# Optimization experiments

Hardware: AMD Instinct MI355X
Metric: run time of the kernel (lower is better)

Reference implementation:

```python
import jax, jax.numpy as jnp
import numpy as np

B, T, DIM = 2, 2048, 2048
H, DH = 16, 128
QC, KVC = 512, 512
DD = 64  # decoupled rope dim


def _rope_freqs(t, dd, theta=10000.0):
    inv = 1.0 / (theta ** (np.arange(0, dd, 2, dtype=np.float32) / dd))  # [dd/2]
    ang = np.arange(t, dtype=np.float32)[:, None] * inv[None, :]         # [T, dd/2]
    return jnp.asarray(np.stack([np.cos(ang), np.sin(ang)], axis=-1))    # [T, dd/2, 2]


def setup_inputs() -> dict:
    key = jax.random.key(0)
    ks = jax.random.split(key, 10)
    def w(k, i, o):
        return jax.random.normal(k, (i, o), jnp.float32) / np.sqrt(i)
    x = jax.random.normal(ks[0], (B, T, DIM), jnp.float32)
    freqs_cis = _rope_freqs(T, DD)
    neg = jnp.float32(-1e9)
    mask = jnp.where(jnp.tril(jnp.ones((T, T), bool)), 0.0, neg).astype(jnp.float32)
    return {
        "x": x, "freqs_cis": freqs_cis, "mask": mask,
        "W_dq": w(ks[1], DIM, QC), "W_uq": w(ks[2], QC, H * DH),
        "W_dkv": w(ks[3], DIM, KVC), "W_uk": w(ks[4], KVC, H * DH),
        "W_uv": w(ks[5], KVC, H * DH), "W_qr": w(ks[6], QC, H * DD),
        "W_kr": w(ks[7], DIM, DD), "W_o": w(ks[8], H * DH, DIM),
    }


def _apply_rope(t, freqs_cis):
    # t: [B, T, H, DD]; freqs_cis: [T, DD/2, 2]
    tp = t.reshape(*t.shape[:-1], -1, 2)               # [B,T,H,DD/2,2]
    cos = freqs_cis[None, :, None, :, 0]
    sin = freqs_cis[None, :, None, :, 1]
    x1, x2 = tp[..., 0], tp[..., 1]
    rot = jnp.stack([x1 * cos - x2 * sin, x1 * sin + x2 * cos], axis=-1)
    return rot.reshape(t.shape)


def reference(x, freqs_cis, mask, W_dq, W_uq, W_dkv, W_uk, W_uv, W_qr, W_kr, W_o):
    q_c = x @ W_dq                                     # [B,T,QC]
    kv_c = x @ W_dkv                                   # [B,T,KVC]
    q_rope = (q_c @ W_qr).reshape(B, T, H, DD)
    kv_rope = jnp.broadcast_to((x @ W_kr)[:, :, None, :], (B, T, H, DD))
    q_rope = _apply_rope(q_rope, freqs_cis)
    kv_rope = _apply_rope(kv_rope, freqs_cis)
    q = (q_c @ W_uq).reshape(B, T, H, DH)
    k = (kv_c @ W_uk).reshape(B, T, H, DH)
    v = (kv_c @ W_uv).reshape(B, T, H, DH)
    q = jnp.concatenate([q, q_rope], axis=-1)          # [B,T,H,DH+DD]
    k = jnp.concatenate([k, kv_rope], axis=-1)
    scale = 1.0 / np.sqrt(DH + DD)
    scores = jnp.einsum("bqhd,bkhd->bhqk", q, k) * scale + mask[None, None]
    attn = jax.nn.softmax(scores, axis=-1)
    out = jnp.einsum("bhqk,bkhd->bqhd", attn, v).reshape(B, T, H * DH)
    return out @ W_o
```

## Files before the change

### kernel.cpp

```cpp
#include <hip/hip_runtime.h>
#include <hip/hip_bf16.h>
#include <cstdint>
#include <cstddef>

typedef __bf16 bf16_t;
typedef __attribute__((ext_vector_type(8))) __bf16 bf16x8;
typedef __attribute__((ext_vector_type(4))) __bf16 bf16x4;
typedef __attribute__((ext_vector_type(4))) float f32x4;

#define B_ 2
#define T_ 2048
#define DIM_ 2048
#define H_ 16
#define DH_ 128
#define DD_ 64
#define DQK_ 192
#define QSTRIDE_ 3072
#define BT_ 4096

__device__ __forceinline__ void gload16(const void* g, void* lds) {
  __builtin_amdgcn_global_load_lds(
      (const __attribute__((address_space(1))) unsigned int*)g,
      (__attribute__((address_space(3))) unsigned int*)lds, 16, 0, 0);
}

struct bf16_4 { bf16_t a, b, c, d; };
__global__ void cast_f32_bf16(const float* __restrict__ in, bf16_t* __restrict__ out, int n4) {
  int i = blockIdx.x * blockDim.x + threadIdx.x;
  if (i >= n4) return;
  float4 v = ((const float4*)in)[i];
  bf16_4 r{(bf16_t)v.x, (bf16_t)v.y, (bf16_t)v.z, (bf16_t)v.w};
  ((bf16_4*)out)[i] = r;
}

__global__ void transpose_all(const float* __restrict__ Wdq, const float* __restrict__ Wdkv,
                              const float* __restrict__ Wkr, const float* __restrict__ Wuq,
                              const float* __restrict__ Wqr, const float* __restrict__ Wuk,
                              const float* __restrict__ Wuv, const float* __restrict__ Wo,
                              bf16_t* __restrict__ Bt1, bf16_t* __restrict__ Bt2,
                              bf16_t* __restrict__ Bt3, bf16_t* __restrict__ Wo_t) {
  __shared__ float tile[32][33];
  int id = blockIdx.x;
  const float* W; bf16_t* Wt; int K, N, Np, kt;
  if (id < 1024)      { W = Wdq;  Wt = Bt1;                          K = 2048; N = 512;  Np = 512;  kt = 64; }
  else if (id < 2048) { W = Wdkv; Wt = Bt1 + (size_t)512 * 2048;  id -= 1024; K = 2048; N = 512;  Np = 512;  kt = 64; }
  else if (id < 2304) { W = Wkr;  Wt = Bt1 + (size_t)1024 * 2048; id -= 2048; K = 2048; N = 64;   Np = 128;  kt = 64; }
  else if (id < 3328) { W = Wuq;  Wt = Bt2;                       id -= 2304; K = 512;  N = 2048; Np = 2048; kt = 16; }
  else if (id < 3840) { W = Wqr;  Wt = Bt2 + (size_t)2048 * 512;  id -= 3328; K = 512;  N = 1024; Np = 1024; kt = 16; }
  else if (id < 4864) { W = Wuk;  Wt = Bt3;                       id -= 3840; K = 512;  N = 2048; Np = 2048; kt = 16; }
  else if (id < 5888) { W = Wuv;  Wt = Bt3 + (size_t)2048 * 512;  id -= 4864; K = 512;  N = 2048; Np = 2048; kt = 16; }
  else                { W = Wo;   Wt = Wo_t;                      id -= 5888; K = 2048; N = 2048; Np = 2048; kt = 64; }
  int k0 = (id % kt) * 32, n0 = (id / kt) * 32;
  int tx = threadIdx.x, ty = threadIdx.y;
#pragma unroll
  for (int i = 0; i < 4; ++i) {
    int k = k0 + ty + i * 8, n = n0 + tx;
    float v = (k < K && n < N) ? W[(size_t)k * N + n] : 0.f;
    tile[ty + i * 8][tx] = v;
  }
  __syncthreads();
#pragma unroll
  for (int i = 0; i < 4; ++i) {
    int n = n0 + ty + i * 8, k = k0 + tx;
    if (n < Np && k < K) Wt[(size_t)n * K + k] = (bf16_t)tile[tx][ty + i * 8];
  }
}

__global__ void transpose_v(const bf16_t* __restrict__ V, bf16_t* __restrict__ Vt) {
  __shared__ bf16_t tile[64 * 64];
  int id = blockIdx.x;
  int t0 = (id & 31) * 64;
  int d0 = ((id >> 5) & 1) * 64;
  int bh = id >> 6;
  int b = bh >> 4, h = bh & 15;
  int t = threadIdx.x;
#pragma unroll
  for (int it = 0; it < 2; ++it) {
    int idx = it * 256 + t;
    int tt = idx >> 3, c = idx & 7;
    bf16x8 v = *(const bf16x8*)&V[(size_t)(b * T_ + t0 + tt) * 2048 + h * 128 + d0 + c * 8];
    int sw = (tt ^ (tt >> 3)) & 7;
    *(bf16x8*)((char*)tile + tt * 128 + 16 * (c ^ sw)) = v;
  }
  __syncthreads();
#pragma unroll
  for (int it = 0; it < 2; ++it) {
    int idx = it * 256 + t;
    int dr = idx >> 3, c = idx & 7;
    bf16_t tmp[8];
#pragma unroll
    for (int u = 0; u < 8; ++u) {
      int sw = (u ^ c) & 7;
      tmp[u] = *(const bf16_t*)((const char*)tile + (8 * c + u) * 128 + ((2 * dr) ^ (16 * sw)));
    }
    *(bf16x8*)&Vt[((size_t)bh * 128 + d0 + dr) * T_ + t0 + c * 8] = *(bf16x8*)tmp;
  }
}

template <int MODE>
__global__ __launch_bounds__(256) void gemm_bt(const bf16_t* __restrict__ A,
                                               const bf16_t* __restrict__ Bt,
                                               void* __restrict__ C0v,
                                               void* __restrict__ C1v,
                                               void* __restrict__ C2v,
                                               const float* __restrict__ fr,
                                               int M, int N, int K, int ldc) {
  __shared__ bf16_t As[128 * 32];
  __shared__ bf16_t Bs[128 * 32];
  const int t = threadIdx.x;
  const int w = t >> 6, l = t & 63, l15 = l & 15, lhi = l >> 4;
  const int m0 = blockIdx.y * 128, n0 = blockIdx.x * 128;
  const int wr = (w >> 1) * 64, wc = (w & 1) * 64;

  f32x4 zero = {0.f, 0.f, 0.f, 0.f};
  f32x4 acc[4][4];
#pragma unroll
  for (int m = 0; m < 4; ++m)
#pragma unroll
    for (int n = 0; n < 4; ++n) acc[m][n] = zero;

  const int e0 = t * 8;
  const int r0 = e0 >> 5, c0 = e0 & 31;
  const int e1 = 2048 + t * 8;
  const int r1 = e1 >> 5, c1 = e1 & 31;

  for (int k0 = 0; k0 < K; k0 += 32) {
    gload16(A + (size_t)(m0 + r0) * K + k0 + c0, &As[e0]);
    gload16(A + (size_t)(m0 + r1) * K + k0 + c1, &As[e1]);
    gload16(Bt + (size_t)(n0 + r0) * K + k0 + c0, &Bs[e0]);
    gload16(Bt + (size_t)(n0 + r1) * K + k0 + c1, &Bs[e1]);
    __syncthreads();
    bf16x8 af[4], bfr[4];
#pragma unroll
    for (int m = 0; m < 4; ++m)
      af[m] = *(const bf16x8*)&As[(wr + m * 16 + l15) * 32 + lhi * 8];
#pragma unroll
    for (int n = 0; n < 4; ++n)
      bfr[n] = *(const bf16x8*)&Bs[(wc + n * 16 + l15) * 32 + lhi * 8];
#pragma unroll
    for (int m = 0; m < 4; ++m)
#pragma unroll
      for (int n = 0; n < 4; ++n)
        acc[m][n] = __builtin_amdgcn_mfma_f32_16x16x32_bf16(af[m], bfr[n], acc[m][n], 0, 0, 0);
    __syncthreads();
  }

#pragma unroll
  for (int m = 0; m < 4; ++m) {
#pragma unroll
    for (int n = 0; n < 4; ++n) {
#pragma unroll
      for (int r = 0; r < 4; ++r) {
        int row = m0 + wr + m * 16 + lhi * 4 + r;
        int col = n0 + wc + n * 16 + l15;
        float v = acc[m][n][r];
        if (MODE == 1) {
          ((float*)C0v)[(size_t)row * ldc + col] = v;
        } else if (MODE == 3) {
          if (col < 512)       ((bf16_t*)C0v)[(size_t)row * 512 + col] = (bf16_t)v;
          else if (col < 1024) ((bf16_t*)C1v)[(size_t)row * 512 + (col - 512)] = (bf16_t)v;
          else if (col < 1088) ((bf16_t*)C2v)[(size_t)row * 64 + (col - 1024)] = (bf16_t)v;
        } else if (MODE == 4) {
          if (col < 2048) {
            ((bf16_t*)C0v)[(size_t)row * QSTRIDE_ + (col >> 7) * DQK_ + (col & 127)] = (bf16_t)v;
          } else {
            float other = __shfl_xor(v, 1, 64);
            int tt = row & (T_ - 1);
            int j = (col & 63) >> 1;
            float2 cs = ((const float2*)fr)[tt * 32 + j];
            float o = (col & 1) ? (other * cs.y + v * cs.x) : (v * cs.x - other * cs.y);
            int hh = (col - 2048) >> 6;
            ((bf16_t*)C0v)[(size_t)row * QSTRIDE_ + hh * DQK_ + 128 + (col & 63)] = (bf16_t)o;
          }
        } else if (MODE == 5) {
          if (col < 2048) ((bf16_t*)C0v)[(size_t)row * QSTRIDE_ + (col >> 7) * DQK_ + (col & 127)] = (bf16_t)v;
          else            ((bf16_t*)C1v)[(size_t)row * 2048 + (col - 2048)] = (bf16_t)v;
        }
      }
    }
  }
}

__global__ void rope_k(const bf16_t* __restrict__ kr, const float* __restrict__ fr,
                       bf16_t* __restrict__ Kb) {
  int idx = blockIdx.x * 256 + threadIdx.x;
  int j = idx & 31;
  int row = idx >> 5;
  int tt = row & (T_ - 1);
  float x1 = (float)kr[(size_t)row * 64 + 2 * j];
  float x2 = (float)kr[(size_t)row * 64 + 2 * j + 1];
  float c = fr[tt * 64 + 2 * j], s = fr[tt * 64 + 2 * j + 1];
  union { bf16_t h2[2]; unsigned u; } pk;
  pk.h2[0] = (bf16_t)(x1 * c - x2 * s);
  pk.h2[1] = (bf16_t)(x1 * s + x2 * c);
#pragma unroll
  for (int h = 0; h < H_; ++h) {
    *(unsigned*)&Kb[(size_t)row * QSTRIDE_ + h * DQK_ + 128 + 2 * j] = pk.u;
  }
}

#define KLDB 200
#define VLDB 72
#define PLDB 68

__global__ __launch_bounds__(256, 2) void flash_attn3(const bf16_t* __restrict__ Q,
                                                      const bf16_t* __restrict__ Kb,
                                                      const bf16_t* __restrict__ Vt,
                                                      bf16_t* __restrict__ Ob) {
  __shared__ bf16_t Ks[64 * KLDB];
  __shared__ bf16_t Vs[128 * VLDB];
  __shared__ bf16_t Ps[4][16 * PLDB];

  const int t = threadIdx.x, w = t >> 6, l = t & 63, l15 = l & 15, lhi = l >> 4;
  const int id = blockIdx.x;
  const int xcd = id & 7, sub = id >> 3;
  const int bh = xcd * 4 + (sub >> 4);
  const int qp = sub & 15;
  const int b = bh >> 4, h = bh & 15;
  const int qa = qp, qb = 31 - qp;
  const float scale = 0.07216878364870322f;

  int rK[6], cK[6];
#pragma unroll
  for (int i = 0; i < 6; ++i) { int idx = i * 256 + t; rK[i] = idx / 24; cK[i] = idx % 24; }
  const int rVt = t >> 3, cV = t & 7;
  const bf16_t* kbase = Kb + (size_t)b * T_ * QSTRIDE_ + h * DQK_;
  const bf16_t* vbase = Vt + (size_t)bh * DH_ * T_;

  bf16x8 kreg[6], vreg[4];
#define LOAD_TILE(K0)                                                                      \
  do {                                                                                     \
    _Pragma("unroll") for (int i = 0; i < 6; ++i)                                          \
        kreg[i] = *(const bf16x8*)(kbase + (size_t)((K0) + rK[i]) * QSTRIDE_ + cK[i] * 8); \
    _Pragma("unroll") for (int i = 0; i < 4; ++i)                                          \
        vreg[i] = *(const bf16x8*)(vbase + (size_t)(i * 32 + rVt) * T_ + (K0) + cV * 8);   \
  } while (0)
#define WRITE_TILE()                                                                       \
  do {                                                                                     \
    _Pragma("unroll") for (int i = 0; i < 6; ++i)                                          \
        *(bf16x8*)&Ks[rK[i] * KLDB + cK[i] * 8] = kreg[i];                                 \
    _Pragma("unroll") for (int i = 0; i < 4; ++i)                                          \
        *(bf16x8*)&Vs[(i * 32 + rVt) * VLDB + cV * 8] = vreg[i];                           \
  } while (0)

  f32x4 zero = {0.f, 0.f, 0.f, 0.f};

  LOAD_TILE(0);
  WRITE_TILE();
  __syncthreads();

  for (int pass = 0; pass < 2; ++pass) {
    const int qt = pass ? qb : qa;

    bf16x8 qf[6];
    {
      const bf16_t* qrow = Q + ((size_t)(b * T_ + qt * 64 + w * 16 + l15)) * QSTRIDE_ + h * DQK_;
#pragma unroll
      for (int kc = 0; kc < 6; ++kc) qf[kc] = *(const bf16x8*)(qrow + kc * 32 + lhi * 8);
    }

    float m_r[4], l_r[4];
    f32x4 accO[8];
#pragma unroll
    for (int r = 0; r < 4; ++r) { m_r[r] = -1e30f; l_r[r] = 0.f; }
#pragma unroll
    for (int n = 0; n < 8; ++n) accO[n] = zero;

    for (int kt = 0; kt <= qt; ++kt) {
      const bool last = (kt == qt);
      const bool haveNext = !(pass == 1 && last);
      if (haveNext) LOAD_TILE(last ? 0 : (kt + 1) * 64);

      f32x4 s[4];
#pragma unroll
      for (int n = 0; n < 4; ++n) s[n] = zero;
      __builtin_amdgcn_s_setprio(1);
#pragma unroll
      for (int kc = 0; kc < 6; ++kc) {
#pragma unroll
        for (int n = 0; n < 4; ++n) {
          bf16x8 kf = *(const bf16x8*)&Ks[(n * 16 + l15) * KLDB + kc * 32 + lhi * 8];
          s[n] = __builtin_amdgcn_mfma_f32_16x16x32_bf16(qf[kc], kf, s[n], 0, 0, 0);
        }
      }
      __builtin_amdgcn_s_setprio(0);

#pragma unroll
      for (int n = 0; n < 4; ++n)
#pragma unroll
        for (int r = 0; r < 4; ++r) {
          float v = s[n][r] * scale;
          if (last) {
            int qq = w * 16 + lhi * 4 + r;
            int kk = n * 16 + l15;
            if (kk > qq) v = -1e30f;
          }
          s[n][r] = v;
        }
      float mn[4], corr[4];
#pragma unroll
      for (int r = 0; r < 4; ++r) {
        float v = fmaxf(fmaxf(s[0][r], s[1][r]), fmaxf(s[2][r], s[3][r]));
#pragma unroll
        for (int off = 1; off < 16; off <<= 1) v = fmaxf(v, __shfl_xor(v, off, 64));
        mn[r] = fmaxf(m_r[r], v);
        corr[r] = __expf(m_r[r] - mn[r]);
        m_r[r] = mn[r];
      }
      float rs[4] = {0.f, 0.f, 0.f, 0.f};
#pragma unroll
      for (int n = 0; n < 4; ++n)
#pragma unroll
        for (int r = 0; r < 4; ++r) {
          float p = __expf(s[n][r] - mn[r]);
          rs[r] += p;
          Ps[w][(lhi * 4 + r) * PLDB + n * 16 + l15] = (bf16_t)p;
        }
#pragma unroll
      for (int r = 0; r < 4; ++r) {
        float v = rs[r];
#pragma unroll
        for (int off = 1; off < 16; off <<= 1) v += __shfl_xor(v, off, 64);
        l_r[r] = l_r[r] * corr[r] + v;
      }
#pragma unroll
      for (int n = 0; n < 8; ++n)
#pragma unroll
        for (int r = 0; r < 4; ++r) accO[n][r] *= corr[r];

      __builtin_amdgcn_s_setprio(1);
#pragma unroll
      for (int kc = 0; kc < 2; ++kc) {
        bf16x4 p0 = *(const bf16x4*)&Ps[w][l15 * PLDB + kc * 32 + lhi * 8];
        bf16x4 p1 = *(const bf16x4*)&Ps[w][l15 * PLDB + kc * 32 + lhi * 8 + 4];
        bf16x8 pf = __builtin_shufflevector(p0, p1, 0, 1, 2, 3, 4, 5, 6, 7);
#pragma unroll
        for (int n = 0; n < 8; ++n) {
          bf16x8 vf = *(const bf16x8*)&Vs[(n * 16 + l15) * VLDB + kc * 32 + lhi * 8];
          accO[n] = __builtin_amdgcn_mfma_f32_16x16x32_bf16(pf, vf, accO[n], 0, 0, 0);
        }
      }
      __builtin_amdgcn_s_setprio(0);

      __syncthreads();
      if (haveNext) WRITE_TILE();
      __syncthreads();
    }

    {
      float inv[4];
#pragma unroll
      for (int r = 0; r < 4; ++r) inv[r] = 1.0f / l_r[r];
#pragma unroll
      for (int n = 0; n < 8; ++n)
#pragma unroll
        for (int r = 0; r < 4; ++r) {
          size_t row = (size_t)(b * T_ + qt * 64 + w * 16 + lhi * 4 + r);
          Ob[row * (H_ * DH_) + h * DH_ + n * 16 + l15] = (bf16_t)(accO[n][r] * inv[r]);
        }
    }
  }
#undef LOAD_TILE
#undef WRITE_TILE
}

extern "C" void kernel_launch(void* const* d_in, const int* in_sizes, int n_in,
                              void* d_out, int out_size, void* d_ws, size_t ws_size,
                              hipStream_t stream) {
  (void)in_sizes; (void)n_in; (void)out_size; (void)ws_size;
  const float* x    = (const float*)d_in[0];
  const float* fr   = (const float*)d_in[1];
  const float* Wdq  = (const float*)d_in[3];
  const float* Wuq  = (const float*)d_in[4];
  const float* Wdkv = (const float*)d_in[5];
  const float* Wuk  = (const float*)d_in[6];
  const float* Wuv  = (const float*)d_in[7];
  const float* Wqr  = (const float*)d_in[8];
  const float* Wkr  = (const float*)d_in[9];
  const float* Wo   = (const float*)d_in[10];
  float* out = (float*)d_out;

  char* ws = (char*)d_ws;
  size_t off = 0;
  auto alloc = [&](size_t bytes) -> void* {
    void* p = ws + off;
    off += (bytes + 255) & ~(size_t)255;
    return p;
  };
  bf16_t* x_bf   = (bf16_t*)alloc((size_t)BT_ * DIM_ * 2);
  bf16_t* Bt1    = (bf16_t*)alloc((size_t)1152 * 2048 * 2);
  bf16_t* Bt2    = (bf16_t*)alloc((size_t)3072 * 512 * 2);
  bf16_t* Bt3    = (bf16_t*)alloc((size_t)4096 * 512 * 2);
  bf16_t* Wo_t   = (bf16_t*)alloc((size_t)2048 * 2048 * 2);
  bf16_t* q_c    = (bf16_t*)alloc((size_t)BT_ * 512 * 2);
  bf16_t* kv_c   = (bf16_t*)alloc((size_t)BT_ * 512 * 2);
  bf16_t* k_rb   = (bf16_t*)alloc((size_t)BT_ * 64 * 2);
  bf16_t* Qbuf   = (bf16_t*)alloc((size_t)BT_ * QSTRIDE_ * 2);
  bf16_t* Kbuf   = (bf16_t*)alloc((size_t)BT_ * QSTRIDE_ * 2);
  bf16_t* Vbuf   = (bf16_t*)alloc((size_t)BT_ * 2048 * 2);
  bf16_t* Vt_g   = (bf16_t*)alloc((size_t)BT_ * 2048 * 2);
  bf16_t* AObuf  = (bf16_t*)alloc((size_t)BT_ * 2048 * 2);

  cast_f32_bf16<<<(BT_ * DIM_ / 4 + 255) / 256, 256, 0, stream>>>(x, x_bf, BT_ * DIM_ / 4);
  transpose_all<<<9984, dim3(32, 8), 0, stream>>>(Wdq, Wdkv, Wkr, Wuq, Wqr, Wuk, Wuv, Wo,
                                                  Bt1, Bt2, Bt3, Wo_t);

  gemm_bt<3><<<dim3(9, 32),  256, 0, stream>>>(x_bf, Bt1, q_c, kv_c, k_rb, nullptr, BT_, 1088, 2048, 0);
  gemm_bt<4><<<dim3(24, 32), 256, 0, stream>>>(q_c,  Bt2, Qbuf, nullptr, nullptr, fr, BT_, 3072, 512, 0);
  gemm_bt<5><<<dim3(32, 32), 256, 0, stream>>>(kv_c, Bt3, Kbuf, Vbuf, nullptr, nullptr, BT_, 4096, 512, 0);

  transpose_v<<<2048, 256, 0, stream>>>(Vbuf, Vt_g);
  rope_k<<<(BT_ * 32) / 256, 256, 0, stream>>>(k_rb, fr, Kbuf);

  flash_attn3<<<512, 256, 0, stream>>>(Qbuf, Kbuf, Vt_g, AObuf);

  gemm_bt<1><<<dim3(16, 32), 256, 0, stream>>>(AObuf, Wo_t, out, nullptr, nullptr, nullptr, BT_, 2048, 2048, 2048);
}
```

Baseline: 318.7 us.

## Fuse prep kernels, K-rope into GEMM epilogue, and V transpose into GEMM

Merges the x cast and the weight transpose into one prep launch. Moves K rope and its 16-head broadcast into the epilogue of the first GEMM. Combines the Q and KV up-projection GEMMs into one launch whose V tiles are transposed through LDS and written straight into Vt. This removes three launches (rope_k, transpose_v, one GEMM) and the round trips through the k_rb and Vbuf intermediates, at the cost of extra LDS and syncs in the V epilogue and more divergence in the epilogues.

```diff
diff --git a/kernel.cpp b/kernel.cpp
--- a/kernel.cpp
+++ b/kernel.cpp
@@ -25,22 +25,24 @@
 }
 
 struct bf16_4 { bf16_t a, b, c, d; };
-__global__ void cast_f32_bf16(const float* __restrict__ in, bf16_t* __restrict__ out, int n4) {
-  int i = blockIdx.x * blockDim.x + threadIdx.x;
-  if (i >= n4) return;
-  float4 v = ((const float4*)in)[i];
-  bf16_4 r{(bf16_t)v.x, (bf16_t)v.y, (bf16_t)v.z, (bf16_t)v.w};
-  ((bf16_4*)out)[i] = r;
-}
-
-__global__ void transpose_all(const float* __restrict__ Wdq, const float* __restrict__ Wdkv,
-                              const float* __restrict__ Wkr, const float* __restrict__ Wuq,
-                              const float* __restrict__ Wqr, const float* __restrict__ Wuk,
-                              const float* __restrict__ Wuv, const float* __restrict__ Wo,
-                              bf16_t* __restrict__ Bt1, bf16_t* __restrict__ Bt2,
-                              bf16_t* __restrict__ Bt3, bf16_t* __restrict__ Wo_t) {
+
+__global__ void prep(const float* __restrict__ x,
+                     const float* __restrict__ Wdq, const float* __restrict__ Wdkv,
+                     const float* __restrict__ Wkr, const float* __restrict__ Wuq,
+                     const float* __restrict__ Wqr, const float* __restrict__ Wuk,
+                     const float* __restrict__ Wuv, const float* __restrict__ Wo,
+                     bf16_t* __restrict__ x_bf,
+                     bf16_t* __restrict__ Bt1, bf16_t* __restrict__ Bt2,
+                     bf16_t* __restrict__ Bt3, bf16_t* __restrict__ Wo_t) {
+  int id = blockIdx.x;
+  if (id >= 9984) {
+    int i = (id - 9984) * 256 + threadIdx.y * 32 + threadIdx.x;
+    float4 v = ((const float4*)x)[i];
+    bf16_4 r{(bf16_t)v.x, (bf16_t)v.y, (bf16_t)v.z, (bf16_t)v.w};
+    ((bf16_4*)x_bf)[i] = r;
+    return;
+  }
   __shared__ float tile[32][33];
-  int id = blockIdx.x;
   const float* W; bf16_t* Wt; int K, N, Np, kt;
   if (id < 1024)      { W = Wdq;  Wt = Bt1;                          K = 2048; N = 512;  Np = 512;  kt = 64; }
   else if (id < 2048) { W = Wdkv; Wt = Bt1 + (size_t)512 * 2048;  id -= 1024; K = 2048; N = 512;  Np = 512;  kt = 64; }
@@ -63,37 +65,6 @@
   for (int i = 0; i < 4; ++i) {
     int n = n0 + ty + i * 8, k = k0 + tx;
     if (n < Np && k < K) Wt[(size_t)n * K + k] = (bf16_t)tile[tx][ty + i * 8];
-  }
-}
-
-__global__ void transpose_v(const bf16_t* __restrict__ V, bf16_t* __restrict__ Vt) {
-  __shared__ bf16_t tile[64 * 64];
-  int id = blockIdx.x;
-  int t0 = (id & 31) * 64;
-  int d0 = ((id >> 5) & 1) * 64;
-  int bh = id >> 6;
-  int b = bh >> 4, h = bh & 15;
-  int t = threadIdx.x;
-#pragma unroll
-  for (int it = 0; it < 2; ++it) {
-    int idx = it * 256 + t;
-    int tt = idx >> 3, c = idx & 7;
-    bf16x8 v = *(const bf16x8*)&V[(size_t)(b * T_ + t0 + tt) * 2048 + h * 128 + d0 + c * 8];
-    int sw = (tt ^ (tt >> 3)) & 7;
-    *(bf16x8*)((char*)tile + tt * 128 + 16 * (c ^ sw)) = v;
-  }
-  __syncthreads();
-#pragma unroll
-  for (int it = 0; it < 2; ++it) {
-    int idx = it * 256 + t;
-    int dr = idx >> 3, c = idx & 7;
-    bf16_t tmp[8];
-#pragma unroll
-    for (int u = 0; u < 8; ++u) {
-      int sw = (u ^ c) & 7;
-      tmp[u] = *(const bf16_t*)((const char*)tile + (8 * c + u) * 128 + ((2 * dr) ^ (16 * sw)));
-    }
-    *(bf16x8*)&Vt[((size_t)bh * 128 + d0 + dr) * T_ + t0 + c * 8] = *(bf16x8*)tmp;
   }
 }
 
@@ -157,45 +128,142 @@
         if (MODE == 1) {
           ((float*)C0v)[(size_t)row * ldc + col] = v;
         } else if (MODE == 3) {
-          if (col < 512)       ((bf16_t*)C0v)[(size_t)row * 512 + col] = (bf16_t)v;
-          else if (col < 1024) ((bf16_t*)C1v)[(size_t)row * 512 + (col - 512)] = (bf16_t)v;
-          else if (col < 1088) ((bf16_t*)C2v)[(size_t)row * 64 + (col - 1024)] = (bf16_t)v;
-        } else if (MODE == 4) {
-          if (col < 2048) {
-            ((bf16_t*)C0v)[(size_t)row * QSTRIDE_ + (col >> 7) * DQK_ + (col & 127)] = (bf16_t)v;
-          } else {
+          if (col < 512) {
+            ((bf16_t*)C0v)[(size_t)row * 512 + col] = (bf16_t)v;
+          } else if (col < 1024) {
+            ((bf16_t*)C1v)[(size_t)row * 512 + (col - 512)] = (bf16_t)v;
+          } else if (col < 1088) {
             float other = __shfl_xor(v, 1, 64);
             int tt = row & (T_ - 1);
-            int j = (col & 63) >> 1;
+            int j = (col - 1024) >> 1;
             float2 cs = ((const float2*)fr)[tt * 32 + j];
             float o = (col & 1) ? (other * cs.y + v * cs.x) : (v * cs.x - other * cs.y);
-            int hh = (col - 2048) >> 6;
-            ((bf16_t*)C0v)[(size_t)row * QSTRIDE_ + hh * DQK_ + 128 + (col & 63)] = (bf16_t)o;
+            float o2 = __shfl_xor(o, 1, 64);
+            if (!(col & 1)) {
+              union { bf16_t h2[2]; unsigned u; } pk;
+              pk.h2[0] = (bf16_t)o;
+              pk.h2[1] = (bf16_t)o2;
+              bf16_t* Kb = (bf16_t*)C2v;
+#pragma unroll
+              for (int hh = 0; hh < H_; ++hh)
+                *(unsigned*)&Kb[(size_t)row * QSTRIDE_ + hh * DQK_ + 128 + (col - 1024)] = pk.u;
+            }
           }
-        } else if (MODE == 5) {
-          if (col < 2048) ((bf16_t*)C0v)[(size_t)row * QSTRIDE_ + (col >> 7) * DQK_ + (col & 127)] = (bf16_t)v;
-          else            ((bf16_t*)C1v)[(size_t)row * 2048 + (col - 2048)] = (bf16_t)v;
-        }
-      }
-    }
-  }
-}
-
-__global__ void rope_k(const bf16_t* __restrict__ kr, const float* __restrict__ fr,
-                       bf16_t* __restrict__ Kb) {
-  int idx = blockIdx.x * 256 + threadIdx.x;
-  int j = idx & 31;
-  int row = idx >> 5;
-  int tt = row & (T_ - 1);
-  float x1 = (float)kr[(size_t)row * 64 + 2 * j];
-  float x2 = (float)kr[(size_t)row * 64 + 2 * j + 1];
-  float c = fr[tt * 64 + 2 * j], s = fr[tt * 64 + 2 * j + 1];
-  union { bf16_t h2[2]; unsigned u; } pk;
-  pk.h2[0] = (bf16_t)(x1 * c - x2 * s);
-  pk.h2[1] = (bf16_t)(x1 * s + x2 * c);
-#pragma unroll
-  for (int h = 0; h < H_; ++h) {
-    *(unsigned*)&Kb[(size_t)row * QSTRIDE_ + h * DQK_ + 128 + 2 * j] = pk.u;
+        }
+      }
+    }
+  }
+}
+
+__global__ __launch_bounds__(256) void gemm45(const bf16_t* __restrict__ q_c,
+                                              const bf16_t* __restrict__ kv_c,
+                                              const bf16_t* __restrict__ Bt2,
+                                              const bf16_t* __restrict__ Bt3,
+                                              bf16_t* __restrict__ Qbuf,
+                                              bf16_t* __restrict__ Kbuf,
+                                              bf16_t* __restrict__ Vt,
+                                              const float* __restrict__ fr) {
+  __shared__ bf16_t As[128 * 32];
+  __shared__ bf16_t Bs[128 * 32];
+  __shared__ bf16_t ctile[64 * 136];
+  const int t = threadIdx.x;
+  const int w = t >> 6, l = t & 63, l15 = l & 15, lhi = l >> 4;
+  const bool isQ = (blockIdx.x < 24);
+  const int bx = isQ ? blockIdx.x : blockIdx.x - 24;
+  const bf16_t* A  = isQ ? q_c : kv_c;
+  const bf16_t* Bt = isQ ? Bt2 : Bt3;
+  constexpr int K = 512;
+  const int m0 = blockIdx.y * 128, n0 = bx * 128;
+  const int wr = (w >> 1) * 64, wc = (w & 1) * 64;
+
+  f32x4 zero = {0.f, 0.f, 0.f, 0.f};
+  f32x4 acc[4][4];
+#pragma unroll
+  for (int m = 0; m < 4; ++m)
+#pragma unroll
+    for (int n = 0; n < 4; ++n) acc[m][n] = zero;
+
+  const int e0 = t * 8;
+  const int r0 = e0 >> 5, c0 = e0 & 31;
+  const int e1 = 2048 + t * 8;
+  const int r1 = e1 >> 5, c1 = e1 & 31;
+
+  for (int k0 = 0; k0 < K; k0 += 32) {
+    gload16(A + (size_t)(m0 + r0) * K + k0 + c0, &As[e0]);
+    gload16(A + (size_t)(m0 + r1) * K + k0 + c1, &As[e1]);
+    gload16(Bt + (size_t)(n0 + r0) * K + k0 + c0, &Bs[e0]);
+    gload16(Bt + (size_t)(n0 + r1) * K + k0 + c1, &Bs[e1]);
+    __syncthreads();
+    bf16x8 af[4], bfr[4];
+#pragma unroll
+    for (int m = 0; m < 4; ++m)
+      af[m] = *(const bf16x8*)&As[(wr + m * 16 + l15) * 32 + lhi * 8];
+#pragma unroll
+    for (int n = 0; n < 4; ++n)
+      bfr[n] = *(const bf16x8*)&Bs[(wc + n * 16 + l15) * 32 + lhi * 8];
+#pragma unroll
+    for (int m = 0; m < 4; ++m)
+#pragma unroll
+      for (int n = 0; n < 4; ++n)
+        acc[m][n] = __builtin_amdgcn_mfma_f32_16x16x32_bf16(af[m], bfr[n], acc[m][n], 0, 0, 0);
+    __syncthreads();
+  }
+
+  const bool isV = (!isQ) && (bx >= 16);
+  if (!isV) {
+#pragma unroll
+    for (int m = 0; m < 4; ++m) {
+#pragma unroll
+      for (int n = 0; n < 4; ++n) {
+#pragma unroll
+        for (int r = 0; r < 4; ++r) {
+          int row = m0 + wr + m * 16 + lhi * 4 + r;
+          int col = n0 + wc + n * 16 + l15;
+          float v = acc[m][n][r];
+          if (isQ) {
+            if (col < 2048) {
+              Qbuf[(size_t)row * QSTRIDE_ + (col >> 7) * DQK_ + (col & 127)] = (bf16_t)v;
+            } else {
+              float other = __shfl_xor(v, 1, 64);
+              int tt = row & (T_ - 1);
+              int j = (col & 63) >> 1;
+              float2 cs = ((const float2*)fr)[tt * 32 + j];
+              float o = (col & 1) ? (other * cs.y + v * cs.x) : (v * cs.x - other * cs.y);
+              int hh = (col - 2048) >> 6;
+              Qbuf[(size_t)row * QSTRIDE_ + hh * DQK_ + 128 + (col & 63)] = (bf16_t)o;
+            }
+          } else {
+            Kbuf[(size_t)row * QSTRIDE_ + (col >> 7) * DQK_ + (col & 127)] = (bf16_t)v;
+          }
+        }
+      }
+    }
+  } else {
+    const int h = bx - 16;
+    const int b = m0 >> 11;
+    const int bh = b * 16 + h;
+    const int tloc = m0 & (T_ - 1);
+#pragma unroll
+    for (int half = 0; half < 2; ++half) {
+      if ((w & 1) == half) {
+#pragma unroll
+        for (int m = 0; m < 4; ++m)
+#pragma unroll
+          for (int n = 0; n < 4; ++n)
+#pragma unroll
+            for (int r = 0; r < 4; ++r)
+              ctile[(n * 16 + l15) * 136 + wr + m * 16 + lhi * 4 + r] = (bf16_t)acc[m][n][r];
+      }
+      __syncthreads();
+#pragma unroll
+      for (int it = 0; it < 4; ++it) {
+        int d = (t >> 4) + it * 16;
+        int t0 = (t & 15) * 8;
+        bf16x8 v = *(const bf16x8*)&ctile[d * 136 + t0];
+        *(bf16x8*)&Vt[((size_t)bh * DH_ + half * 64 + d) * T_ + tloc + t0] = v;
+      }
+      __syncthreads();
+    }
   }
 }
 
@@ -394,23 +462,17 @@
   bf16_t* Wo_t   = (bf16_t*)alloc((size_t)2048 * 2048 * 2);
   bf16_t* q_c    = (bf16_t*)alloc((size_t)BT_ * 512 * 2);
   bf16_t* kv_c   = (bf16_t*)alloc((size_t)BT_ * 512 * 2);
-  bf16_t* k_rb   = (bf16_t*)alloc((size_t)BT_ * 64 * 2);
   bf16_t* Qbuf   = (bf16_t*)alloc((size_t)BT_ * QSTRIDE_ * 2);
   bf16_t* Kbuf   = (bf16_t*)alloc((size_t)BT_ * QSTRIDE_ * 2);
-  bf16_t* Vbuf   = (bf16_t*)alloc((size_t)BT_ * 2048 * 2);
   bf16_t* Vt_g   = (bf16_t*)alloc((size_t)BT_ * 2048 * 2);
   bf16_t* AObuf  = (bf16_t*)alloc((size_t)BT_ * 2048 * 2);
 
-  cast_f32_bf16<<<(BT_ * DIM_ / 4 + 255) / 256, 256, 0, stream>>>(x, x_bf, BT_ * DIM_ / 4);
-  transpose_all<<<9984, dim3(32, 8), 0, stream>>>(Wdq, Wdkv, Wkr, Wuq, Wqr, Wuk, Wuv, Wo,
-                                                  Bt1, Bt2, Bt3, Wo_t);
-
-  gemm_bt<3><<<dim3(9, 32),  256, 0, stream>>>(x_bf, Bt1, q_c, kv_c, k_rb, nullptr, BT_, 1088, 2048, 0);
-  gemm_bt<4><<<dim3(24, 32), 256, 0, stream>>>(q_c,  Bt2, Qbuf, nullptr, nullptr, fr, BT_, 3072, 512, 0);
-  gemm_bt<5><<<dim3(32, 32), 256, 0, stream>>>(kv_c, Bt3, Kbuf, Vbuf, nullptr, nullptr, BT_, 4096, 512, 0);
-
-  transpose_v<<<2048, 256, 0, stream>>>(Vbuf, Vt_g);
-  rope_k<<<(BT_ * 32) / 256, 256, 0, stream>>>(k_rb, fr, Kbuf);
+  prep<<<18176, dim3(32, 8), 0, stream>>>(x, Wdq, Wdkv, Wkr, Wuq, Wqr, Wuk, Wuv, Wo,
+                                          x_bf, Bt1, Bt2, Bt3, Wo_t);
+
+  gemm_bt<3><<<dim3(9, 32), 256, 0, stream>>>(x_bf, Bt1, q_c, kv_c, Kbuf, fr, BT_, 1088, 2048, 0);
+
+  gemm45<<<dim3(56, 32), 256, 0, stream>>>(q_c, kv_c, Bt2, Bt3, Qbuf, Kbuf, Vt_g, fr);
 
   flash_attn3<<<512, 256, 0, stream>>>(Qbuf, Kbuf, Vt_g, AObuf);
 
```

New measurement: 324.2 us. Within noise of the previous version (+1.7%).
